# Kernel tuning notes

Measured on AMD Instinct MI355X. Metric: run time of the kernel, lower is better.

The kernel has to match this reference:

```python
import jax, jax.numpy as jnp
import numpy as np

N_NODES = 100000
N_EDGES = 1600000
IN_DIM = 512
HID = 32
BN_EPS = 1e-5


def _gcn_layer(x, W, b, src, dst, n_nodes):
    # GCNConv: x' = D^{-1/2} (A + I) D^{-1/2} (x W) + b, degrees include self-loop
    h = x @ W  # [N, H]
    deg = jax.ops.segment_sum(jnp.ones(src.shape[0], x.dtype), dst, num_segments=n_nodes) + 1.0
    dinv = jax.lax.rsqrt(deg)  # [N]
    coef = dinv[src] * dinv[dst]  # [E]
    msg = h[src] * coef[:, None]  # gather + scale, [E, H]
    agg = jax.ops.segment_sum(msg, dst, num_segments=n_nodes)  # scatter-add
    agg = agg + h * (dinv * dinv)[:, None]  # self-loop term
    return agg + b


def setup_inputs() -> dict:
    key = jax.random.key(0)
    ks = jax.random.split(key, 10)
    x = jax.random.normal(ks[0], (N_NODES, IN_DIM), dtype=jnp.float32)
    edge_index = jax.random.randint(ks[1], (2, N_EDGES), 0, N_NODES, dtype=jnp.int32)
    W1 = jax.random.normal(ks[2], (IN_DIM, HID), dtype=jnp.float32) / np.sqrt(IN_DIM)
    b1 = jnp.zeros((HID,), jnp.float32)
    W2 = jax.random.normal(ks[3], (HID, HID), dtype=jnp.float32) / np.sqrt(HID)
    b2 = jnp.zeros((HID,), jnp.float32)
    gamma = jnp.ones((HID,), jnp.float32)
    beta = jnp.zeros((HID,), jnp.float32)
    run_mean = jnp.zeros((HID,), jnp.float32)
    run_var = jnp.ones((HID,), jnp.float32)
    return {"x": x, "edge_index": edge_index, "W1": W1, "b1": b1, "W2": W2,
            "b2": b2, "gamma": gamma, "beta": beta, "run_mean": run_mean, "run_var": run_var}


def reference(x, edge_index, W1, b1, W2, b2, gamma, beta, run_mean, run_var):
    # Eval mode: dropout is identity, BatchNorm uses running stats.
    src, dst = edge_index[0], edge_index[1]
    h = _gcn_layer(x, W1, b1, src, dst, N_NODES)
    h = jax.nn.relu(h)
    h = (h - run_mean) * jax.lax.rsqrt(run_var + BN_EPS) * gamma + beta
    h = _gcn_layer(h, W2, b2, src, dst, N_NODES)
    h = jax.nn.relu(h)
    return h  # post_process is undefined in source -> identity
```

## Files before the change

kernel.cpp:

```cpp
#include <hip/hip_runtime.h>

#define NN 100000
#define NE 1600000
#define IN_DIM 512
#define HID 32
#define BN_EPS 1e-5f

#define E_PER 4
#define FILL_BLOCKS 1600
#define GEMM_BLOCKS 782
#define FG_BLOCKS (FILL_BLOCKS + GEMM_BLOCKS)
#define NPASS 25
#define SEG 64

__global__ void k_zero(int* __restrict__ p, int n) {
    int i = blockIdx.x * 256 + threadIdx.x;
    if (i < n) p[i] = 0;
}

__device__ inline void fma4(float4& a, float s, const float4& w) {
    a.x = fmaf(s, w.x, a.x);
    a.y = fmaf(s, w.y, a.y);
    a.z = fmaf(s, w.z, a.z);
    a.w = fmaf(s, w.w, a.w);
}

#define XS_S 132
__global__ __launch_bounds__(256) void k_fill_gemm(const int* __restrict__ src,
                                                   const int* __restrict__ dst,
                                                   int* __restrict__ cnt,
                                                   int* __restrict__ csr,
                                                   const float* __restrict__ x,
                                                   const float* __restrict__ W,
                                                   float* __restrict__ h) {
    __shared__ float XsT[32 * XS_S];
    __shared__ float Ws[32 * 32];
    int bid = blockIdx.x;
    int t = threadIdx.x;
    bool is_gemm = (bid % 3 == 2) && (bid / 3 < GEMM_BLOCKS);

    if (!is_gemm) {
        int f = bid - min(GEMM_BLOCKS, (bid + 1) / 3);
        const int nthreads = FILL_BLOCKS * 256;
        int tid = f * 256 + t;
        int s[E_PER], d[E_PER];
#pragma unroll
        for (int k = 0; k < E_PER; k++) {
            int e = tid + k * nthreads;
            bool ok = (e < NE);
            s[k] = ok ? src[e] : 0;
            d[k] = ok ? dst[e] : -1;
        }
        for (int p = 0; p < NPASS; p++) {
#pragma unroll
            for (int k = 0; k < E_PER; k++) {
                if ((d[k] >> 12) == p) {
                    int pos = atomicAdd(&cnt[d[k]], 1);
                    if (pos < SEG) csr[d[k] * SEG + pos] = s[k];
                }
            }
        }
        return;
    }

    int g = bid / 3;
    int tc = t & 7;
    int tr = t >> 3;
    int base = g * 128;

    float4 acc[4] = {{0,0,0,0},{0,0,0,0},{0,0,0,0},{0,0,0,0}};
    int st_c4 = t & 7, st_row = t >> 3;

    for (int kt = 0; kt < IN_DIM; kt += 32) {
        __syncthreads();
#pragma unroll
        for (int i = 0; i < 4; i++) {
            int row = st_row + i * 32;
            int gr = min(base + row, NN - 1);
            float4 v = *(const float4*)(x + (size_t)gr * IN_DIM + kt + (st_c4 << 2));
            XsT[(st_c4 * 4 + 0) * XS_S + row] = v.x;
            XsT[(st_c4 * 4 + 1) * XS_S + row] = v.y;
            XsT[(st_c4 * 4 + 2) * XS_S + row] = v.z;
            XsT[(st_c4 * 4 + 3) * XS_S + row] = v.w;
        }
        *(float4*)&Ws[t * 4] = *(const float4*)(W + kt * HID + t * 4);
        __syncthreads();

#pragma unroll
        for (int kk = 0; kk < 32; kk++) {
            float4 xv = *(const float4*)&XsT[kk * XS_S + tr * 4];
            float4 wv = *(const float4*)&Ws[kk * HID + tc * 4];
            fma4(acc[0], xv.x, wv);
            fma4(acc[1], xv.y, wv);
            fma4(acc[2], xv.z, wv);
            fma4(acc[3], xv.w, wv);
        }
    }
#pragma unroll
    for (int r = 0; r < 4; r++) {
        int row = base + tr * 4 + r;
        if (row < NN) *(float4*)(h + (size_t)row * HID + (tc << 2)) = acc[r];
    }
}

__global__ __launch_bounds__(256) void k_agg1(const float* __restrict__ h,
                                              const int* __restrict__ csr,
                                              const int* __restrict__ cnt,
                                              const float* __restrict__ bias,
                                              const float* __restrict__ gamma,
                                              const float* __restrict__ beta,
                                              const float* __restrict__ mean,
                                              const float* __restrict__ var,
                                              float* __restrict__ h2, int n) {
    int t = threadIdx.x;
    int c = t & 31;
    int node = blockIdx.x * 8 + (t >> 5);
    if (node >= n) return;

    int dnode = cnt[node];
    float dn = rsqrtf((float)dnode + 1.0f);
    int d = min(dnode, SEG);
    int o0 = node * SEG;
    float sum = h[(size_t)node * HID + c] * dn;

    for (int ch = 0; ch < d; ch += 32) {
        int rem = d - ch;
        int sv = 0;
        float dv = 0.f;
        if (c < rem) {
            sv = csr[o0 + ch + c];
            dv = rsqrtf((float)cnt[sv] + 1.0f);
        }
        int m = min(rem, 32);
        int mu = (m + 7) & ~7;
        for (int j = 0; j < mu; j += 8) {
            int ss[8];
            float cf[8], v[8];
#pragma unroll
            for (int u = 0; u < 8; u++) {
                ss[u] = __shfl(sv, j + u, 32);
                cf[u] = __shfl(dv, j + u, 32);
            }
#pragma unroll
            for (int u = 0; u < 8; u++) v[u] = h[(size_t)ss[u] * HID + c];
#pragma unroll
            for (int u = 0; u < 8; u++) sum = fmaf(v[u], cf[u], sum);
        }
    }
    float acc = sum * dn;
    float v = fmaxf(acc + bias[c], 0.0f);
    v = (v - mean[c]) * rsqrtf(var[c] + BN_EPS) * gamma[c] + beta[c];
    h2[(size_t)node * HID + c] = v;
}

__global__ __launch_bounds__(256) void k_agg2(const float* __restrict__ h2,
                                              const int* __restrict__ csr,
                                              const int* __restrict__ cnt,
                                              const float* __restrict__ W2,
                                              const float* __restrict__ b2,
                                              float* __restrict__ out, int n) {
    __shared__ float W2s[32 * 32];
    int t = threadIdx.x;
    ((float4*)W2s)[t] = ((const float4*)W2)[t];
    __syncthreads();

    int c = t & 31;
    int node = blockIdx.x * 8 + (t >> 5);
    if (node >= n) return;

    int dnode = cnt[node];
    float dn = rsqrtf((float)dnode + 1.0f);
    int d = min(dnode, SEG);
    int o0 = node * SEG;
    float sum = h2[(size_t)node * HID + c] * dn;

    for (int ch = 0; ch < d; ch += 32) {
        int rem = d - ch;
        int sv = 0;
        float dv = 0.f;
        if (c < rem) {
            sv = csr[o0 + ch + c];
            dv = rsqrtf((float)cnt[sv] + 1.0f);
        }
        int m = min(rem, 32);
        int mu = (m + 7) & ~7;
        for (int j = 0; j < mu; j += 8) {
            int ss[8];
            float cf[8], v[8];
#pragma unroll
            for (int u = 0; u < 8; u++) {
                ss[u] = __shfl(sv, j + u, 32);
                cf[u] = __shfl(dv, j + u, 32);
            }
#pragma unroll
            for (int u = 0; u < 8; u++) v[u] = h2[(size_t)ss[u] * HID + c];
#pragma unroll
            for (int u = 0; u < 8; u++) sum = fmaf(v[u], cf[u], sum);
        }
    }
    float acc = sum * dn;
    float g = 0.f;
#pragma unroll
    for (int cc = 0; cc < 32; cc++) {
        float a = __shfl(acc, cc, 32);
        g = fmaf(a, W2s[cc * HID + c], g);
    }
    out[(size_t)node * HID + c] = fmaxf(g + b2[c], 0.0f);
}

extern "C" void kernel_launch(void* const* d_in, const int* in_sizes, int n_in,
                              void* d_out, int out_size, void* d_ws, size_t ws_size,
                              hipStream_t stream) {
    const float* x     = (const float*)d_in[0];
    const int*   ei    = (const int*)d_in[1];
    const int*   src   = ei;
    const int*   dst   = ei + NE;
    const float* W1    = (const float*)d_in[2];
    const float* b1    = (const float*)d_in[3];
    const float* W2    = (const float*)d_in[4];
    const float* b2    = (const float*)d_in[5];
    const float* gamma = (const float*)d_in[6];
    const float* beta  = (const float*)d_in[7];
    const float* rmean = (const float*)d_in[8];
    const float* rvar  = (const float*)d_in[9];
    float* out = (float*)d_out;

    char* ws = (char*)d_ws;
    int*   cnt = (int*)(ws);
    int*   csr = (int*)(ws + ((size_t)1 << 20));
    float* h1  = (float*)(ws + ((size_t)28 << 20));
    float* h2  = (float*)(ws + ((size_t)42 << 20));

    k_zero<<<(NN + 255) / 256, 256, 0, stream>>>(cnt, NN);
    k_fill_gemm<<<FG_BLOCKS, 256, 0, stream>>>(src, dst, cnt, csr, x, W1, h1);
    k_agg1<<<(NN + 7) / 8, 256, 0, stream>>>(h1, csr, cnt, b1, gamma, beta,
                                             rmean, rvar, h2, NN);
    k_agg2<<<(NN + 7) / 8, 256, 0, stream>>>(h2, csr, cnt, W2, b2, out, NN);
}
```

Baseline: 464.4 us.

## Pre-scale node features by source degree norm to drop per-edge cnt gathers

Folds the source-side D^{-1/2} factor into the node features before aggregation. A new scale kernel produces a pre-scaled layer-1 input, and layer 1 writes its output already scaled for layer 2. The aggregation loops become plain sums, so the random gather of cnt[src] and the rsqrt per edge are gone. A zero padding row at index n stands in for masked lanes. The cost is an extra kernel launch and an extra pass over the 12.8MB feature array.

```diff
diff --git a/kernel.cpp b/kernel.cpp
--- a/kernel.cpp
+++ b/kernel.cpp
@@ -103,7 +103,22 @@
     }
 }
 
-__global__ __launch_bounds__(256) void k_agg1(const float* __restrict__ h,
+__global__ __launch_bounds__(256) void k_scale(const float* __restrict__ h1,
+                                               const int* __restrict__ cnt,
+                                               float* __restrict__ h1s) {
+    int idx = blockIdx.x * 256 + threadIdx.x;
+    if (idx >= (NN + 1) * 8) return;
+    int row = idx >> 3, c4 = idx & 7;
+    float4 v = {0.f, 0.f, 0.f, 0.f};
+    if (row < NN) {
+        float dn = rsqrtf((float)cnt[row] + 1.0f);
+        float4 a = ((const float4*)(h1 + (size_t)row * HID))[c4];
+        v.x = a.x * dn; v.y = a.y * dn; v.z = a.z * dn; v.w = a.w * dn;
+    }
+    ((float4*)(h1s + (size_t)row * HID))[c4] = v;
+}
+
+__global__ __launch_bounds__(256) void k_agg1(const float* __restrict__ hs,
                                               const int* __restrict__ csr,
                                               const int* __restrict__ cnt,
                                               const float* __restrict__ bias,
@@ -111,49 +126,45 @@
                                               const float* __restrict__ beta,
                                               const float* __restrict__ mean,
                                               const float* __restrict__ var,
-                                              float* __restrict__ h2, int n) {
+                                              float* __restrict__ h2s, int n) {
     int t = threadIdx.x;
     int c = t & 31;
     int node = blockIdx.x * 8 + (t >> 5);
-    if (node >= n) return;
+    if (node > n) return;
+    if (node == n) {
+        h2s[(size_t)n * HID + c] = 0.f;
+        return;
+    }
 
     int dnode = cnt[node];
     float dn = rsqrtf((float)dnode + 1.0f);
     int d = min(dnode, SEG);
     int o0 = node * SEG;
-    float sum = h[(size_t)node * HID + c] * dn;
+    float sum = hs[(size_t)node * HID + c];
 
     for (int ch = 0; ch < d; ch += 32) {
         int rem = d - ch;
-        int sv = 0;
-        float dv = 0.f;
-        if (c < rem) {
-            sv = csr[o0 + ch + c];
-            dv = rsqrtf((float)cnt[sv] + 1.0f);
-        }
+        int sv = (c < rem) ? csr[o0 + ch + c] : n;
         int m = min(rem, 32);
         int mu = (m + 7) & ~7;
         for (int j = 0; j < mu; j += 8) {
             int ss[8];
-            float cf[8], v[8];
-#pragma unroll
-            for (int u = 0; u < 8; u++) {
-                ss[u] = __shfl(sv, j + u, 32);
-                cf[u] = __shfl(dv, j + u, 32);
-            }
-#pragma unroll
-            for (int u = 0; u < 8; u++) v[u] = h[(size_t)ss[u] * HID + c];
-#pragma unroll
-            for (int u = 0; u < 8; u++) sum = fmaf(v[u], cf[u], sum);
+            float v[8];
+#pragma unroll
+            for (int u = 0; u < 8; u++) ss[u] = __shfl(sv, j + u, 32);
+#pragma unroll
+            for (int u = 0; u < 8; u++) v[u] = hs[(size_t)ss[u] * HID + c];
+#pragma unroll
+            for (int u = 0; u < 8; u++) sum += v[u];
         }
     }
     float acc = sum * dn;
     float v = fmaxf(acc + bias[c], 0.0f);
     v = (v - mean[c]) * rsqrtf(var[c] + BN_EPS) * gamma[c] + beta[c];
-    h2[(size_t)node * HID + c] = v;
-}
-
-__global__ __launch_bounds__(256) void k_agg2(const float* __restrict__ h2,
+    h2s[(size_t)node * HID + c] = v * dn;
+}
+
+__global__ __launch_bounds__(256) void k_agg2(const float* __restrict__ h2s,
                                               const int* __restrict__ csr,
                                               const int* __restrict__ cnt,
                                               const float* __restrict__ W2,
@@ -172,30 +183,22 @@
     float dn = rsqrtf((float)dnode + 1.0f);
     int d = min(dnode, SEG);
     int o0 = node * SEG;
-    float sum = h2[(size_t)node * HID + c] * dn;
+    float sum = h2s[(size_t)node * HID + c];
 
     for (int ch = 0; ch < d; ch += 32) {
         int rem = d - ch;
-        int sv = 0;
-        float dv = 0.f;
-        if (c < rem) {
-            sv = csr[o0 + ch + c];
-            dv = rsqrtf((float)cnt[sv] + 1.0f);
-        }
+        int sv = (c < rem) ? csr[o0 + ch + c] : n;
         int m = min(rem, 32);
         int mu = (m + 7) & ~7;
         for (int j = 0; j < mu; j += 8) {
             int ss[8];
-            float cf[8], v[8];
-#pragma unroll
-            for (int u = 0; u < 8; u++) {
-                ss[u] = __shfl(sv, j + u, 32);
-                cf[u] = __shfl(dv, j + u, 32);
-            }
-#pragma unroll
-            for (int u = 0; u < 8; u++) v[u] = h2[(size_t)ss[u] * HID + c];
-#pragma unroll
-            for (int u = 0; u < 8; u++) sum = fmaf(v[u], cf[u], sum);
+            float v[8];
+#pragma unroll
+            for (int u = 0; u < 8; u++) ss[u] = __shfl(sv, j + u, 32);
+#pragma unroll
+            for (int u = 0; u < 8; u++) v[u] = h2s[(size_t)ss[u] * HID + c];
+#pragma unroll
+            for (int u = 0; u < 8; u++) sum += v[u];
         }
     }
     float acc = sum * dn;
@@ -229,11 +232,13 @@
     int*   cnt = (int*)(ws);
     int*   csr = (int*)(ws + ((size_t)1 << 20));
     float* h1  = (float*)(ws + ((size_t)28 << 20));
-    float* h2  = (float*)(ws + ((size_t)42 << 20));
+    float* h1s = (float*)(ws + ((size_t)42 << 20));
+    float* h2s = (float*)(ws + ((size_t)56 << 20));
 
     k_zero<<<(NN + 255) / 256, 256, 0, stream>>>(cnt, NN);
     k_fill_gemm<<<FG_BLOCKS, 256, 0, stream>>>(src, dst, cnt, csr, x, W1, h1);
-    k_agg1<<<(NN + 7) / 8, 256, 0, stream>>>(h1, csr, cnt, b1, gamma, beta,
-                                             rmean, rvar, h2, NN);
-    k_agg2<<<(NN + 7) / 8, 256, 0, stream>>>(h2, csr, cnt, W2, b2, out, NN);
-}
+    k_scale<<<((NN + 1) * 8 + 255) / 256, 256, 0, stream>>>(h1, cnt, h1s);
+    k_agg1<<<(NN + 1 + 7) / 8, 256, 0, stream>>>(h1s, csr, cnt, b1, gamma, beta,
+                                                 rmean, rvar, h2s, NN);
+    k_agg2<<<(NN + 7) / 8, 256, 0, stream>>>(h2s, csr, cnt, W2, b2, out, NN);
+}
```

Result: no change. 456.2 us (-1.8%).
